# Performance work log

Hardware: AMD Instinct MI355X
Metric: run time of the kernel (lower is better)

The kernel has to match this reference:

```python
import jax, jax.numpy as jnp
import numpy as np

B, S, DIM = 4, 2048, 1024
E, K, H = 8, 2, 2048


def setup_inputs() -> dict:
    key = jax.random.key(0)
    ks = jax.random.split(key, 4)
    def init(k, shp, fan_in):
        return (jax.random.normal(k, shp, jnp.float32) / np.sqrt(fan_in)).astype(jnp.float32)
    return {
        "x": jax.random.normal(ks[0], (B, S, DIM), jnp.float32),
        "gate_w": init(ks[1], (DIM, E), DIM),
        "gate_b": jnp.zeros((E,), jnp.float32),
        "w1": init(ks[2], (E, DIM, H), DIM),
        "b1": jnp.zeros((E, H), jnp.float32),
        "w2": init(ks[3], (E, H, DIM), H),
        "b2": jnp.zeros((E, DIM), jnp.float32),
    }


def reference(x, gate_w, gate_b, w1, b1, w2, b2):
    orig_shape = x.shape
    xt = x.reshape(-1, orig_shape[-1])           # [N, D]
    N = xt.shape[0]

    logits = xt @ gate_w + gate_b                # [N, E]
    gate_weights = jax.nn.softmax(logits, axis=-1)
    top_w, top_i = jax.lax.top_k(gate_weights, K)           # [N, K]
    top_w = top_w / top_w.sum(axis=-1, keepdims=True)

    # combine weights: comb[n, e] = sum_k top_w[n,k] * (top_i[n,k] == e)
    comb = jnp.zeros((N, E), xt.dtype).at[jnp.arange(N)[:, None], top_i].add(top_w)

    # dense all-expert FFN (same math as masked gather/scatter loop)
    h = jax.nn.relu(jnp.einsum('nd,edh->neh', xt, w1) + b1)   # [N, E, H]
    out_e = jnp.einsum('neh,ehd->ned', h, w2) + b2            # [N, E, D]
    final = jnp.einsum('ne,ned->nd', comb, out_e).reshape(orig_shape)

    # load balancing loss
    usage = jnp.sum(jax.nn.one_hot(top_i, E, dtype=xt.dtype), axis=1)  # [N, E]
    expert_router_prob = gate_weights.sum(axis=0) / N
    expert_fraction_routed = usage.sum(axis=0) / N
    load_balancing_loss = jnp.sum(expert_router_prob * expert_fraction_routed)

    return final, load_balancing_loss
```

## Files before the change

### kernel.cpp

```cpp
#include <hip/hip_runtime.h>
#include <hip/hip_fp16.h>
#include <stdint.h>

#define N_TOK 8192
#define DIMD 1024
#define NEXP 8
#define HDIM 2048
#define BM 128
#define BN 128
#define BKK 64
#define MAXTILES 136
#define MAXROWS (MAXTILES * BM)
#define DUMPROW (2 * N_TOK)
#define CAP1 320
#define CAP2 160
#define G1 (8 * CAP1 + MAXTILES * 16)
#define G2 (8 * CAP2 + MAXTILES * 8)
#define TRB1 4096
#define TW2 4096

typedef __attribute__((ext_vector_type(8))) short short8;
typedef __attribute__((ext_vector_type(4))) float f32x4;

__device__ __forceinline__ ushort f2bf(float f) {
    uint32_t u = __float_as_uint(f);
    u += 0x7fffu + ((u >> 16) & 1u);
    return (ushort)(u >> 16);
}

__device__ __forceinline__ void gload_lds16(const void* gsrc, void* lds_dst) {
    __builtin_amdgcn_global_load_lds(
        (const __attribute__((address_space(1))) void*)(uintptr_t)(gsrc),
        (__attribute__((address_space(3))) void*)(uintptr_t)(lds_dst),
        16, 0, 0);
}

__device__ __forceinline__ bool slot_map(const int* __restrict__ counts, int s,
                                         int NB, int CAP,
                                         int* e_out, int* tm_out, int* nb_out) {
    int ec[8], es[8], tot = 0;
#pragma unroll
    for (int e = 0; e < 8; e++) { es[e] = tot; ec[e] = (counts[e] + 127) >> 7; tot += ec[e]; }
    int aff = 8 * CAP;
    if (s < aff) {
        int e = s & 7, j = s >> 3;
        int need = ec[e] * NB;
        int lim = need < CAP ? need : CAP;
        if (j >= lim) return false;
        *e_out = e; *tm_out = es[e] + j / NB; *nb_out = j % NB;
        return true;
    }
    int O = s - aff, acc = 0;
#pragma unroll
    for (int e = 0; e < 8; e++) {
        int over = ec[e] * NB - CAP; if (over < 0) over = 0;
        if (O < acc + over) {
            int j = CAP + (O - acc);
            *e_out = e; *tm_out = es[e] + j / NB; *nb_out = j % NB;
            return true;
        }
        acc += over;
    }
    return false;
}

__device__ __forceinline__ void transpose_tile(const float* __restrict__ pin,
                                               ushort* __restrict__ pout,
                                               int R, int C, int rt, int ct,
                                               float (*t)[65], int tid) {
    int lr = tid >> 4, lc4 = (tid & 15) * 4;
#pragma unroll
    for (int i = 0; i < 4; i++) {
        int r = lr + i * 16;
        const float4 v = *(const float4*)(pin + (size_t)(rt * 64 + r) * C + ct * 64 + lc4);
        t[r][lc4] = v.x; t[r][lc4 + 1] = v.y; t[r][lc4 + 2] = v.z; t[r][lc4 + 3] = v.w;
    }
    __syncthreads();
    int c = tid >> 2, rs = (tid & 3) * 16;
    alignas(16) ushort tmp[16];
#pragma unroll
    for (int j = 0; j < 16; j++) tmp[j] = f2bf(t[rs + j][c]);
    ushort* dst = pout + (size_t)(ct * 64 + c) * R + rt * 64 + rs;
    *(short8*)(dst) = *(const short8*)(tmp);
    *(short8*)(dst + 8) = *(const short8*)(tmp + 8);
}


__global__ void prep_kernel(const float* __restrict__ w1, ushort* __restrict__ w1t,
                            const float* __restrict__ x, const float* __restrict__ gw,
                            const float* __restrict__ gb, int* __restrict__ topi,
                            float* __restrict__ topw, int* __restrict__ counts,
                            float* __restrict__ probsum, ushort* __restrict__ xb,
                            int* __restrict__ row_token, float* __restrict__ row_weight) {
    __shared__ float t[64][65];
    int tid = threadIdx.x;
    if (blockIdx.x < TRB1) {
        int id = blockIdx.x;
        int e = id >> 9, tt = id & 511;
        int ctiles = HDIM >> 6;
        int rt = tt / ctiles, ct = tt % ctiles;
        transpose_tile(w1 + (size_t)e * DIMD * HDIM, w1t + (size_t)e * DIMD * HDIM,
                       DIMD, HDIM, rt, ct, t, tid);
        return;
    }
    int gid = blockIdx.x - TRB1;
    float* ps = (float*)t;
    int* cs = (int*)(t + 1);
    if (gid < MAXROWS / 256) {
        int i = gid * 256 + tid;
        row_token[i] = DUMPROW; row_weight[i] = 0.f;
    }
    if (tid < NEXP) { ps[tid] = 0.f; cs[tid] = 0; }
    __syncthreads();
    int wid = tid >> 6, lane = tid & 63;
    int n = gid * 4 + wid;
    const float* xr = x + (size_t)n * DIMD;
    ushort* xbr = xb + (size_t)n * DIMD;
    float acc[NEXP];
#pragma unroll
    for (int e = 0; e < NEXP; e++) acc[e] = 0.f;
    for (int i = 0; i < DIMD / 64; i++) {
        int c = lane + i * 64;
        float xv = xr[c];
        xbr[c] = f2bf(xv);
        const float* g = gw + (size_t)c * NEXP;
#pragma unroll
        for (int e = 0; e < NEXP; e++) acc[e] += xv * g[e];
    }
#pragma unroll
    for (int e = 0; e < NEXP; e++) {
        float v = acc[e];
#pragma unroll
        for (int off = 32; off > 0; off >>= 1) v += __shfl_xor(v, off);
        acc[e] = v + gb[e];
    }
    float m = acc[0];
#pragma unroll
    for (int e = 1; e < NEXP; e++) m = fmaxf(m, acc[e]);
    float p[NEXP], s = 0.f;
#pragma unroll
    for (int e = 0; e < NEXP; e++) { p[e] = expf(acc[e] - m); s += p[e]; }
    int e1 = 0;
#pragma unroll
    for (int e = 1; e < NEXP; e++) if (p[e] > p[e1]) e1 = e;
    int e2 = (e1 == 0) ? 1 : 0;
#pragma unroll
    for (int e = 0; e < NEXP; e++) if (e != e1 && p[e] > p[e2]) e2 = e;
    float wa = p[e1] / (p[e1] + p[e2]);
    if (lane == 0) {
        topi[n * 2] = e1; topi[n * 2 + 1] = e2;
        topw[n * 2] = wa; topw[n * 2 + 1] = 1.f - wa;
        atomicAdd(&cs[e1], 1); atomicAdd(&cs[e2], 1);
        float inv = 1.f / s;
#pragma unroll
        for (int e = 0; e < NEXP; e++) atomicAdd(&ps[e], p[e] * inv);
    }
    __syncthreads();
    if (tid < NEXP) { atomicAdd(&probsum[tid], ps[tid]); atomicAdd(&counts[tid], cs[tid]); }
}


__global__ void scatter_kernel(const int* __restrict__ topi, const float* __restrict__ topw,
                               const int* __restrict__ counts, int* __restrict__ cursor,
                               int* __restrict__ row_token, float* __restrict__ row_weight) {
    __shared__ int lcnt[NEXP], lbase[NEXP];
    int t = blockIdx.x * 256 + threadIdx.x;
    if (threadIdx.x < NEXP) lcnt[threadIdx.x] = 0;
    __syncthreads();
    int e = topi[t];
    int lpos = atomicAdd(&lcnt[e], 1);
    __syncthreads();
    if (threadIdx.x < NEXP) lbase[threadIdx.x] = atomicAdd(&cursor[threadIdx.x], lcnt[threadIdx.x]);
    __syncthreads();
    int pb = 0;
#pragma unroll
    for (int q = 0; q < NEXP; q++) {
        int rounded = ((counts[q] + 127) >> 7) << 7;
        pb += (q < e) ? rounded : 0;
    }
    int pos = pb + lbase[e] + lpos;
    row_token[pos] = t;
    row_weight[pos] = topw[t];
}


__global__ __launch_bounds__(256, 3) void gemm1_kernel(
        const ushort* __restrict__ xb, const ushort* __restrict__ w1t,
        const float* __restrict__ b1, ushort* __restrict__ hbuf,
        const int* __restrict__ row_token, const int* __restrict__ counts,
        const float* __restrict__ w2, ushort* __restrict__ w2t) {
    __shared__ alignas(16) ushort ldsA[BM * BKK];
    __shared__ alignas(16) ushort ldsB[BN * BKK];
    __shared__ float t[64][65];
    int tid = threadIdx.x;
    if (blockIdx.x < TW2) {
        int id = blockIdx.x;
        int e = id >> 9, tt = id & 511;
        int ctiles = DIMD >> 6;
        int rt = tt / ctiles, ct = tt % ctiles;
        transpose_tile(w2 + (size_t)e * HDIM * DIMD, w2t + (size_t)e * HDIM * DIMD,
                       HDIM, DIMD, rt, ct, t, tid);
        return;
    }
    int e, tm, nb;
    if (!slot_map(counts, blockIdx.x - TW2, 16, CAP1, &e, &tm, &nb)) return;
    int nbase = nb * BN;
    int slotbase = tm * BM;
    int lane = tid & 63, wid = tid >> 6;
    int wr = wid >> 1, wc = wid & 1;
    f32x4 acc[4][4];
#pragma unroll
    for (int i = 0; i < 4; i++)
#pragma unroll
        for (int j = 0; j < 4; j++) acc[i][j] = (f32x4){0.f, 0.f, 0.f, 0.f};
    int arow[4], acol[4], tok[4];
#pragma unroll
    for (int i = 0; i < 4; i++) {
        int p = i * 4096 + wid * 1024 + lane * 16;
        int row = p >> 7;
        int srclo = (p & 127) ^ ((row & 7) << 4);
        arow[i] = row; acol[i] = srclo >> 1;
        tok[i] = row_token[slotbase + row] >> 1;
    }
    const ushort* bmat = w1t + (size_t)e * HDIM * DIMD;
    const int NT = DIMD / BKK;

#pragma unroll
    for (int i = 0; i < 4; i++) {
        gload_lds16(xb + (size_t)tok[i] * DIMD + acol[i], &ldsA[i * 2048 + wid * 512]);
        gload_lds16(bmat + (size_t)(nbase + arow[i]) * DIMD + acol[i],
                    &ldsB[i * 2048 + wid * 512]);
    }
    __syncthreads();

    for (int kt = 0; kt < NT; kt++) {
        short8 af[4][2], bfv[4][2];
#pragma unroll
        for (int kk = 0; kk < 2; kk++) {
#pragma unroll
            for (int im = 0; im < 4; im++) {
                int row = wr * 64 + im * 16 + (lane & 15);
                int kbyte = kk * 64 + ((lane >> 4) * 16);
                af[im][kk] = *(const short8*)((const char*)ldsA +
                              row * 128 + (kbyte ^ ((row & 7) << 4)));
            }
#pragma unroll
            for (int in = 0; in < 4; in++) {
                int row = wc * 64 + in * 16 + (lane & 15);
                int kbyte = kk * 64 + ((lane >> 4) * 16);
                bfv[in][kk] = *(const short8*)((const char*)ldsB +
                               row * 128 + (kbyte ^ ((row & 7) << 4)));
            }
        }
        __syncthreads();
        if (kt + 1 < NT) {
            int k0 = (kt + 1) * BKK;
#pragma unroll
            for (int i = 0; i < 4; i++) {
                gload_lds16(xb + (size_t)tok[i] * DIMD + k0 + acol[i],
                            &ldsA[i * 2048 + wid * 512]);
                gload_lds16(bmat + (size_t)(nbase + arow[i]) * DIMD + k0 + acol[i],
                            &ldsB[i * 2048 + wid * 512]);
            }
        }
        __builtin_amdgcn_sched_barrier(0);
#pragma unroll
        for (int kk = 0; kk < 2; kk++)
#pragma unroll
            for (int im = 0; im < 4; im++)
#pragma unroll
                for (int in = 0; in < 4; in++)
                    acc[im][in] = __builtin_amdgcn_mfma_f32_16x16x32_bf16(
                        af[im][kk], bfv[in][kk], acc[im][in], 0, 0, 0);
        __syncthreads();
    }
    const float* b1e = b1 + (size_t)e * HDIM;
#pragma unroll
    for (int im = 0; im < 4; im++) {
#pragma unroll
        for (int in = 0; in < 4; in++) {
            int col = nbase + wc * 64 + in * 16 + (lane & 15);
            float bias = b1e[col];
#pragma unroll
            for (int r = 0; r < 4; r++) {
                int row = slotbase + wr * 64 + im * 16 + (lane >> 4) * 4 + r;
                float v = fmaxf(acc[im][in][r] + bias, 0.f);
                hbuf[(size_t)row * HDIM + col] = f2bf(v);
            }
        }
    }
}

__global__ __launch_bounds__(256, 3) void gemm2_kernel(
        const ushort* __restrict__ hbuf, const ushort* __restrict__ w2t,
        const float* __restrict__ b2, __half* __restrict__ pairbuf,
        const int* __restrict__ row_token, const float* __restrict__ row_weight,
        const int* __restrict__ counts) {
    int e, tm, nb;
    if (!slot_map(counts, blockIdx.x, 8, CAP2, &e, &tm, &nb)) return;
    int nbase = nb * BN;
    int slotbase = tm * BM;
    __shared__ alignas(16) ushort ldsA[BM * BKK];
    __shared__ alignas(16) ushort ldsB[BN * BKK];
    int tid = threadIdx.x, lane = tid & 63, wid = tid >> 6;
    int wr = wid >> 1, wc = wid & 1;
    f32x4 acc[4][4];
#pragma unroll
    for (int i = 0; i < 4; i++)
#pragma unroll
        for (int j = 0; j < 4; j++) acc[i][j] = (f32x4){0.f, 0.f, 0.f, 0.f};
    int arow[4], acol[4];
#pragma unroll
    for (int i = 0; i < 4; i++) {
        int p = i * 4096 + wid * 1024 + lane * 16;
        int row = p >> 7;
        int srclo = (p & 127) ^ ((row & 7) << 4);
        arow[i] = row; acol[i] = srclo >> 1;
    }
    const ushort* amat = hbuf + (size_t)slotbase * HDIM;
    const ushort* bmat = w2t + (size_t)e * DIMD * HDIM;
    const int NT = HDIM / BKK;

#pragma unroll
    for (int i = 0; i < 4; i++) {
        gload_lds16(amat + (size_t)arow[i] * HDIM + acol[i], &ldsA[i * 2048 + wid * 512]);
        gload_lds16(bmat + (size_t)(nbase + arow[i]) * HDIM + acol[i],
                    &ldsB[i * 2048 + wid * 512]);
    }
    __syncthreads();

    for (int kt = 0; kt < NT; kt++) {
        short8 af[4][2], bfv[4][2];
#pragma unroll
        for (int kk = 0; kk < 2; kk++) {
#pragma unroll
            for (int im = 0; im < 4; im++) {
                int row = wr * 64 + im * 16 + (lane & 15);
                int kbyte = kk * 64 + ((lane >> 4) * 16);
                af[im][kk] = *(const short8*)((const char*)ldsA +
                              row * 128 + (kbyte ^ ((row & 7) << 4)));
            }
#pragma unroll
            for (int in = 0; in < 4; in++) {
                int row = wc * 64 + in * 16 + (lane & 15);
                int kbyte = kk * 64 + ((lane >> 4) * 16);
                bfv[in][kk] = *(const short8*)((const char*)ldsB +
                               row * 128 + (kbyte ^ ((row & 7) << 4)));
            }
        }
        __syncthreads();
        if (kt + 1 < NT) {
            int k0 = (kt + 1) * BKK;
#pragma unroll
            for (int i = 0; i < 4; i++) {
                gload_lds16(amat + (size_t)arow[i] * HDIM + k0 + acol[i],
                            &ldsA[i * 2048 + wid * 512]);
                gload_lds16(bmat + (size_t)(nbase + arow[i]) * HDIM + k0 + acol[i],
                            &ldsB[i * 2048 + wid * 512]);
            }
        }
        __builtin_amdgcn_sched_barrier(0);
#pragma unroll
        for (int kk = 0; kk < 2; kk++)
#pragma unroll
            for (int im = 0; im < 4; im++)
#pragma unroll
                for (int in = 0; in < 4; in++)
                    acc[im][in] = __builtin_amdgcn_mfma_f32_16x16x32_bf16(
                        af[im][kk], bfv[in][kk], acc[im][in], 0, 0, 0);
        __syncthreads();
    }
    const float* b2e = b2 + (size_t)e * DIMD;
#pragma unroll
    for (int im = 0; im < 4; im++) {
#pragma unroll
        for (int r = 0; r < 4; r++) {
            int srow = slotbase + wr * 64 + im * 16 + (lane >> 4) * 4 + r;
            int pair = row_token[srow];
            float w = row_weight[srow];
            __half* prow = pairbuf + (size_t)pair * DIMD;
#pragma unroll
            for (int in = 0; in < 4; in++) {
                int col = nbase + wc * 64 + in * 16 + (lane & 15);
                float v = acc[im][in][r] + b2e[col];
                prow[col] = __float2half(w * v);
            }
        }
    }
}

__global__ void combine_kernel(const __half* __restrict__ pairbuf, float* __restrict__ outp,
                               const float* __restrict__ probsum, const int* __restrict__ counts) {
    int i = blockIdx.x * blockDim.x + threadIdx.x;
    int o = i * 8;
    int t = o >> 10, d = o & 1023;
    const __half* p0 = pairbuf + ((size_t)(t * 2) << 10) + d;
    const __half* p1 = p0 + DIMD;
    short8 h0 = *(const short8*)p0;
    short8 h1 = *(const short8*)p1;
    float4 r0, r1;
#pragma unroll
    for (int j = 0; j < 4; j++) {
        ((float*)&r0)[j] = __half2float(__ushort_as_half((ushort)h0[j])) +
                           __half2float(__ushort_as_half((ushort)h1[j]));
        ((float*)&r1)[j] = __half2float(__ushort_as_half((ushort)h0[j + 4])) +
                           __half2float(__ushort_as_half((ushort)h1[j + 4]));
    }
    float4* dst = (float4*)(outp + o);
    dst[0] = r0; dst[1] = r1;
    if (i == 0) {
        float l = 0.f;
#pragma unroll
        for (int e = 0; e < NEXP; e++) l += probsum[e] * (float)counts[e];
        outp[(size_t)N_TOK * DIMD] = l / ((float)N_TOK * (float)N_TOK);
    }
}


extern "C" void kernel_launch(void* const* d_in, const int* in_sizes, int n_in,
                              void* d_out, int out_size, void* d_ws, size_t ws_size,
                              hipStream_t stream) {
    const float* x      = (const float*)d_in[0];
    const float* gate_w = (const float*)d_in[1];
    const float* gate_b = (const float*)d_in[2];
    const float* w1     = (const float*)d_in[3];
    const float* b1     = (const float*)d_in[4];
    const float* w2     = (const float*)d_in[5];
    const float* b2     = (const float*)d_in[6];
    float* outp = (float*)d_out;

    char* ws = (char*)d_ws;
    ushort* xb   = (ushort*)(ws);
    ushort* w1t  = (ushort*)(ws + 16777216);
    ushort* w2t  = (ushort*)(ws + 50331648);
    ushort* hbuf = (ushort*)(ws + 83886080);
    __half* pairbuf = (__half*)(ws);
    char* ctrl   = ws + 155189248;
    int*   counts     = (int*)(ctrl + 0);
    int*   cursor     = (int*)(ctrl + 32);
    float* probsum    = (float*)(ctrl + 64);
    int*   topi       = (int*)(ctrl + 2048);
    float* topw       = (float*)(ctrl + 2048 + 65536);
    int*   row_token  = (int*)(ctrl + 2048 + 131072);
    float* row_weight = (float*)(ctrl + 2048 + 131072 + 69632);

    hipMemsetAsync(ctrl, 0, 128, stream);

    prep_kernel<<<TRB1 + N_TOK / 4, 256, 0, stream>>>(w1, w1t, x, gate_w, gate_b,
                                                      topi, topw, counts, probsum, xb,
                                                      row_token, row_weight);
    scatter_kernel<<<(N_TOK * 2) / 256, 256, 0, stream>>>(topi, topw, counts, cursor,
                                                          row_token, row_weight);
    gemm1_kernel<<<TW2 + G1, 256, 0, stream>>>(xb, w1t, b1, hbuf, row_token, counts,
                                               w2, w2t);
    gemm2_kernel<<<G2, 256, 0, stream>>>(hbuf, w2t, b2, pairbuf, row_token, row_weight, counts);
    combine_kernel<<<(N_TOK * DIMD / 8) / 256, 256, 0, stream>>>(pairbuf, outp,
                                                                 probsum, counts);
}
```

Before: 233.1 us.

## Enlarge weight transpose tiles, union LDS, and move w2 transpose after GEMM1 blocks

The weight-transpose tiles grow from 64x64 to 64x128, which halves the transpose block count and gives each thread more work. GEMM1 and the transpose now share one LDS buffer instead of allocating both, which lowers the kernel's LDS footprint. The w2 transpose blocks are moved to the end of the gemm1 grid, so the GEMM blocks are dispatched first and the transposes fill in behind them. The gate-weight loads in the router are also vectorised to float4. The risk is that the larger per-block LDS for the transpose, and its new position in the grid, could change occupancy or create tail effects.

Result: no change. 230.6 us, median of 2 (-1.1%).

```diff
diff --git a/kernel.cpp b/kernel.cpp
--- a/kernel.cpp
+++ b/kernel.cpp
@@ -16,8 +16,9 @@
 #define CAP2 160
 #define G1 (8 * CAP1 + MAXTILES * 16)
 #define G2 (8 * CAP2 + MAXTILES * 8)
-#define TRB1 4096
-#define TW2 4096
+#define TRB1 2048
+#define TW2 2048
+#define SMEM_BYTES 33024
 
 typedef __attribute__((ext_vector_type(8))) short short8;
 typedef __attribute__((ext_vector_type(4))) float f32x4;
@@ -67,22 +68,24 @@
 __device__ __forceinline__ void transpose_tile(const float* __restrict__ pin,
                                                ushort* __restrict__ pout,
                                                int R, int C, int rt, int ct,
-                                               float (*t)[65], int tid) {
-    int lr = tid >> 4, lc4 = (tid & 15) * 4;
-#pragma unroll
-    for (int i = 0; i < 4; i++) {
-        int r = lr + i * 16;
-        const float4 v = *(const float4*)(pin + (size_t)(rt * 64 + r) * C + ct * 64 + lc4);
-        t[r][lc4] = v.x; t[r][lc4 + 1] = v.y; t[r][lc4 + 2] = v.z; t[r][lc4 + 3] = v.w;
-    }
-    __syncthreads();
-    int c = tid >> 2, rs = (tid & 3) * 16;
-    alignas(16) ushort tmp[16];
-#pragma unroll
-    for (int j = 0; j < 16; j++) tmp[j] = f2bf(t[rs + j][c]);
-    ushort* dst = pout + (size_t)(ct * 64 + c) * R + rt * 64 + rs;
-    *(short8*)(dst) = *(const short8*)(tmp);
-    *(short8*)(dst + 8) = *(const short8*)(tmp + 8);
+                                               float (*t)[129], int tid) {
+#pragma unroll
+    for (int k = 0; k < 8; k++) {
+        int q = tid + k * 256;
+        int r = q >> 5, c4 = (q & 31) * 4;
+        const float4 v = *(const float4*)(pin + (size_t)(rt * 64 + r) * C + ct * 128 + c4);
+        t[r][c4] = v.x; t[r][c4 + 1] = v.y; t[r][c4 + 2] = v.z; t[r][c4 + 3] = v.w;
+    }
+    __syncthreads();
+#pragma unroll
+    for (int k = 0; k < 4; k++) {
+        int p = tid + k * 256;
+        int c = p >> 3, rs = (p & 7) * 8;
+        alignas(16) ushort tmp[8];
+#pragma unroll
+        for (int j = 0; j < 8; j++) tmp[j] = f2bf(t[rs + j][c]);
+        *(short8*)(pout + (size_t)(ct * 128 + c) * R + rt * 64 + rs) = *(const short8*)tmp;
+    }
 }
 
 
@@ -92,20 +95,19 @@
                             float* __restrict__ topw, int* __restrict__ counts,
                             float* __restrict__ probsum, ushort* __restrict__ xb,
                             int* __restrict__ row_token, float* __restrict__ row_weight) {
-    __shared__ float t[64][65];
+    __shared__ alignas(16) char smem[SMEM_BYTES];
     int tid = threadIdx.x;
     if (blockIdx.x < TRB1) {
         int id = blockIdx.x;
-        int e = id >> 9, tt = id & 511;
-        int ctiles = HDIM >> 6;
-        int rt = tt / ctiles, ct = tt % ctiles;
+        int e = id >> 8, tt = id & 255;
+        int rt = tt >> 4, ct = tt & 15;
         transpose_tile(w1 + (size_t)e * DIMD * HDIM, w1t + (size_t)e * DIMD * HDIM,
-                       DIMD, HDIM, rt, ct, t, tid);
+                       DIMD, HDIM, rt, ct, (float(*)[129])smem, tid);
         return;
     }
     int gid = blockIdx.x - TRB1;
-    float* ps = (float*)t;
-    int* cs = (int*)(t + 1);
+    float* ps = (float*)smem;
+    int* cs = (int*)(smem + 64);
     if (gid < MAXROWS / 256) {
         int i = gid * 256 + tid;
         row_token[i] = DUMPROW; row_weight[i] = 0.f;
@@ -123,9 +125,12 @@
         int c = lane + i * 64;
         float xv = xr[c];
         xbr[c] = f2bf(xv);
-        const float* g = gw + (size_t)c * NEXP;
-#pragma unroll
-        for (int e = 0; e < NEXP; e++) acc[e] += xv * g[e];
+        const float4* g4 = (const float4*)(gw + (size_t)c * NEXP);
+        float4 ga = g4[0], gbv = g4[1];
+        acc[0] += xv * ga.x;  acc[1] += xv * ga.y;
+        acc[2] += xv * ga.z;  acc[3] += xv * ga.w;
+        acc[4] += xv * gbv.x; acc[5] += xv * gbv.y;
+        acc[6] += xv * gbv.z; acc[7] += xv * gbv.w;
     }
 #pragma unroll
     for (int e = 0; e < NEXP; e++) {
@@ -189,21 +194,20 @@
         const float* __restrict__ b1, ushort* __restrict__ hbuf,
         const int* __restrict__ row_token, const int* __restrict__ counts,
         const float* __restrict__ w2, ushort* __restrict__ w2t) {
-    __shared__ alignas(16) ushort ldsA[BM * BKK];
-    __shared__ alignas(16) ushort ldsB[BN * BKK];
-    __shared__ float t[64][65];
+    __shared__ alignas(16) char smem[SMEM_BYTES];
+    ushort* ldsA = (ushort*)smem;
+    ushort* ldsB = (ushort*)(smem + 16384);
     int tid = threadIdx.x;
-    if (blockIdx.x < TW2) {
-        int id = blockIdx.x;
-        int e = id >> 9, tt = id & 511;
-        int ctiles = DIMD >> 6;
-        int rt = tt / ctiles, ct = tt % ctiles;
+    if (blockIdx.x >= G1) {
+        int id = blockIdx.x - G1;
+        int e = id >> 8, tt = id & 255;
+        int rt = tt >> 3, ct = tt & 7;
         transpose_tile(w2 + (size_t)e * HDIM * DIMD, w2t + (size_t)e * HDIM * DIMD,
-                       HDIM, DIMD, rt, ct, t, tid);
+                       HDIM, DIMD, rt, ct, (float(*)[129])smem, tid);
         return;
     }
     int e, tm, nb;
-    if (!slot_map(counts, blockIdx.x - TW2, 16, CAP1, &e, &tm, &nb)) return;
+    if (!slot_map(counts, blockIdx.x, 16, CAP1, &e, &tm, &nb)) return;
     int nbase = nb * BN;
     int slotbase = tm * BM;
     int lane = tid & 63, wid = tid >> 6;
@@ -227,9 +231,9 @@
 
 #pragma unroll
     for (int i = 0; i < 4; i++) {
-        gload_lds16(xb + (size_t)tok[i] * DIMD + acol[i], &ldsA[i * 2048 + wid * 512]);
+        gload_lds16(xb + (size_t)tok[i] * DIMD + acol[i], ldsA + i * 2048 + wid * 512);
         gload_lds16(bmat + (size_t)(nbase + arow[i]) * DIMD + acol[i],
-                    &ldsB[i * 2048 + wid * 512]);
+                    ldsB + i * 2048 + wid * 512);
     }
     __syncthreads();
 
@@ -258,9 +262,9 @@
 #pragma unroll
             for (int i = 0; i < 4; i++) {
                 gload_lds16(xb + (size_t)tok[i] * DIMD + k0 + acol[i],
-                            &ldsA[i * 2048 + wid * 512]);
+                            ldsA + i * 2048 + wid * 512);
                 gload_lds16(bmat + (size_t)(nbase + arow[i]) * DIMD + k0 + acol[i],
-                            &ldsB[i * 2048 + wid * 512]);
+                            ldsB + i * 2048 + wid * 512);
             }
         }
         __builtin_amdgcn_sched_barrier(0);
@@ -451,7 +455,7 @@
                                                       row_token, row_weight);
     scatter_kernel<<<(N_TOK * 2) / 256, 256, 0, stream>>>(topi, topw, counts, cursor,
                                                           row_token, row_weight);
-    gemm1_kernel<<<TW2 + G1, 256, 0, stream>>>(xb, w1t, b1, hbuf, row_token, counts,
+    gemm1_kernel<<<G1 + TW2, 256, 0, stream>>>(xb, w1t, b1, hbuf, row_token, counts,
                                                w2, w2t);
     gemm2_kernel<<<G2, 256, 0, stream>>>(hbuf, w2t, b2, pairbuf, row_token, row_weight, counts);
     combine_kernel<<<(N_TOK * DIMD / 8) / 256, 256, 0, stream>>>(pairbuf, outp,
```
